# Performance work log

Measured on AMD Instinct MI355X. Metric: run time of the kernel, lower is better.

Reference implementation:

```python
import jax, jax.numpy as jnp
import numpy as np

N, CIN, H, W_ = 16, 64, 56, 56
COUT, K, STRIDE, PAD = 64, 3, 1, 1


def setup_inputs() -> dict:
    key = jax.random.key(0)
    k1, k2 = jax.random.split(key)
    x = jax.random.normal(k1, (N, CIN, H, W_), dtype=jnp.float32)
    adder = jax.random.normal(k2, (COUT, CIN, K, K), dtype=jnp.float32)
    return {"x": x, "adder": adder}


def reference(x, adder):
    # AdderNet 2d: out[n,co,h,w] = -sum_{ci,kh,kw} |patch(n,:,h,w) - adder[co]|
    n, c, h, w = x.shape
    co = adder.shape[0]
    # im2col: [N, C*K*K, Ho, Wo]; feature dim ordered (c, kh, kw), matching
    # torch.nn.functional.unfold and adder.reshape(Co, C*K*K).
    patches = jax.lax.conv_general_dilated_patches(
        x, filter_shape=(K, K), window_strides=(STRIDE, STRIDE),
        padding=((PAD, PAD), (PAD, PAD)))
    n_, ckk, ho, wo = patches.shape
    p = patches.reshape(n_, ckk, ho * wo)          # [N, CKK, L]
    w_col = adder.reshape(co, ckk)                 # [Co, CKK]

    def per_filter(wf):
        # wf: [CKK]; negative L1 distance of this filter to every patch
        return -jnp.sum(jnp.abs(p - wf[None, :, None]), axis=1)  # [N, L]

    # Sequential map over output channels avoids materializing the full
    # [Co, N, CKK, L] broadcast tensor (~7 GB); peak extra memory is one
    # [N, CKK, L] diff buffer per step.
    out = jax.lax.map(per_filter, w_col)           # [Co, N, L]
    out = out.transpose(1, 0, 2).reshape(n_, co, ho, wo)
    return out
```

## Files before the change

### kernel.cpp

```cpp
#include <hip/hip_runtime.h>

#define N_    16
#define CIN_  64
#define HW_   56
#define COUT_ 64
#define HP    58
#define HPSQ  (HP * HP)

typedef float f4u __attribute__((ext_vector_type(4), aligned(4)));

__global__ void pad_x_kernel(const float* __restrict__ x, float* __restrict__ xp) {
    int idx = blockIdx.x * 256 + threadIdx.x;
    const int total = N_ * CIN_ * HPSQ;
    if (idx >= total) return;
    int w  = idx % HP;
    int t  = idx / HP;
    int h  = t % HP;
    int nc = t / HP;
    float v = 0.f;
    if (h >= 1 && h <= HW_ && w >= 1 && w <= HW_)
        v = x[((size_t)nc * HW_ + (h - 1)) * HW_ + (w - 1)];
    xp[idx] = v;
}

__device__ __forceinline__ void load_tile(const float* __restrict__ xc,
                                          float (&buf)[9][9]) {
    #pragma unroll
    for (int r = 0; r < 9; ++r) {
        f4u a = *(const f4u*)(xc + r * HP);
        f4u b = *(const f4u*)(xc + r * HP + 4);
        float c = xc[r * HP + 8];
        buf[r][0] = a.x; buf[r][1] = a.y; buf[r][2] = a.z; buf[r][3] = a.w;
        buf[r][4] = b.x; buf[r][5] = b.y; buf[r][6] = b.z; buf[r][7] = b.w;
        buf[r][8] = c;
    }
}

__device__ __forceinline__ void compute_tile(const float* __restrict__ wci,
                                             const float (&buf)[9][9],
                                             float (&acc)[7][7]) {
    #pragma unroll
    for (int kh = 0; kh < 3; ++kh) {
        #pragma unroll
        for (int kw = 0; kw < 3; ++kw) {
            float wv = wci[kh * 3 + kw];
            #pragma unroll
            for (int oh = 0; oh < 7; ++oh)
                #pragma unroll
                for (int j = 0; j < 7; ++j)
                    acc[oh][j] += fabsf(buf[oh + kh][j + kw] - wv);
        }
    }
}

__global__ __launch_bounds__(128, 2) void adder_main_kernel(
    const float* __restrict__ xp, const float* __restrict__ wt,
    float* __restrict__ out) {
    __shared__ float red[64][49];

    int bid  = blockIdx.x;
    int n    = bid >> 6;
    int co   = bid & 63;
    int tid  = threadIdx.x;
    int wid  = tid >> 6;
    int lane = tid & 63;
    int tx   = lane & 7;
    int ty   = lane >> 3;
    int h0   = ty * 7;
    int w0   = tx * 7;

    const float* xbase = xp + (size_t)n * CIN_ * HPSQ + h0 * HP + w0;
    const float* wbase = wt + co * 576;

    float acc[7][7];
    #pragma unroll
    for (int oh = 0; oh < 7; ++oh)
        #pragma unroll
        for (int j = 0; j < 7; ++j) acc[oh][j] = 0.f;

    const int ci0 = wid * 32;
    for (int ci = ci0; ci < ci0 + 32; ++ci) {
        float buf[9][9];
        load_tile(xbase + (size_t)ci * HPSQ, buf);
        compute_tile(wbase + ci * 9, buf, acc);
    }

    if (wid == 1) {
        #pragma unroll
        for (int oh = 0; oh < 7; ++oh)
            #pragma unroll
            for (int j = 0; j < 7; ++j) red[lane][oh * 7 + j] = acc[oh][j];
    }
    __syncthreads();
    if (wid == 0) {
        float* ob = out + ((size_t)(n * COUT_ + co) * HW_ + h0) * HW_ + w0;
        #pragma unroll
        for (int oh = 0; oh < 7; ++oh)
            #pragma unroll
            for (int j = 0; j < 7; ++j)
                ob[oh * HW_ + j] = -(acc[oh][j] + red[lane][oh * 7 + j]);
    }
}

extern "C" void kernel_launch(void* const* d_in, const int* in_sizes, int n_in,
                              void* d_out, int out_size, void* d_ws, size_t ws_size,
                              hipStream_t stream) {
    const float* x     = (const float*)d_in[0];
    const float* adder = (const float*)d_in[1];
    float* out = (float*)d_out;

    float* xp = (float*)d_ws;

    const int padTotal = N_ * CIN_ * HPSQ;
    pad_x_kernel<<<(padTotal + 255) / 256, 256, 0, stream>>>(x, xp);
    adder_main_kernel<<<N_ * COUT_, 128, 0, stream>>>(xp, adder, out);
}
```

Baseline: 211.5 us.

## Split input channels across four wavefronts and interleave row loads with compute

New measurement: 187.8 us. 1.13x faster.

```diff
diff --git a/kernel.cpp b/kernel.cpp
--- a/kernel.cpp
+++ b/kernel.cpp
@@ -23,40 +23,10 @@
     xp[idx] = v;
 }
 
-__device__ __forceinline__ void load_tile(const float* __restrict__ xc,
-                                          float (&buf)[9][9]) {
-    #pragma unroll
-    for (int r = 0; r < 9; ++r) {
-        f4u a = *(const f4u*)(xc + r * HP);
-        f4u b = *(const f4u*)(xc + r * HP + 4);
-        float c = xc[r * HP + 8];
-        buf[r][0] = a.x; buf[r][1] = a.y; buf[r][2] = a.z; buf[r][3] = a.w;
-        buf[r][4] = b.x; buf[r][5] = b.y; buf[r][6] = b.z; buf[r][7] = b.w;
-        buf[r][8] = c;
-    }
-}
-
-__device__ __forceinline__ void compute_tile(const float* __restrict__ wci,
-                                             const float (&buf)[9][9],
-                                             float (&acc)[7][7]) {
-    #pragma unroll
-    for (int kh = 0; kh < 3; ++kh) {
-        #pragma unroll
-        for (int kw = 0; kw < 3; ++kw) {
-            float wv = wci[kh * 3 + kw];
-            #pragma unroll
-            for (int oh = 0; oh < 7; ++oh)
-                #pragma unroll
-                for (int j = 0; j < 7; ++j)
-                    acc[oh][j] += fabsf(buf[oh + kh][j + kw] - wv);
-        }
-    }
-}
-
-__global__ __launch_bounds__(128, 2) void adder_main_kernel(
+__global__ __launch_bounds__(256, 4) void adder_main_kernel(
     const float* __restrict__ xp, const float* __restrict__ wt,
     float* __restrict__ out) {
-    __shared__ float red[64][49];
+    __shared__ float red[3][64][49];
 
     int bid  = blockIdx.x;
     int n    = bid >> 6;
@@ -70,35 +40,68 @@
     int w0   = tx * 7;
 
     const float* xbase = xp + (size_t)n * CIN_ * HPSQ + h0 * HP + w0;
-    const float* wbase = wt + co * 576;
+    const float* wbase = wt + (size_t)co * 576;
 
-    float acc[7][7];
-    #pragma unroll
-    for (int oh = 0; oh < 7; ++oh)
+    float acc[7][7] = {};
+
+    const int ci0 = wid * 16;
+    for (int ci = ci0; ci < ci0 + 16; ++ci) {
+        const float* xc  = xbase + (size_t)ci * HPSQ;
+        const float* wci = wbase + ci * 9;
+        float w[9];
         #pragma unroll
-        for (int j = 0; j < 7; ++j) acc[oh][j] = 0.f;
+        for (int k = 0; k < 9; ++k) w[k] = wci[k];
 
-    const int ci0 = wid * 32;
-    for (int ci = ci0; ci < ci0 + 32; ++ci) {
         float buf[9][9];
-        load_tile(xbase + (size_t)ci * HPSQ, buf);
-        compute_tile(wbase + ci * 9, buf, acc);
+        #define LOADROW(r) { \
+            f4u a_ = *(const f4u*)(xc + (r) * HP);      \
+            f4u b_ = *(const f4u*)(xc + (r) * HP + 4);  \
+            buf[r][0] = a_.x; buf[r][1] = a_.y; buf[r][2] = a_.z; buf[r][3] = a_.w; \
+            buf[r][4] = b_.x; buf[r][5] = b_.y; buf[r][6] = b_.z; buf[r][7] = b_.w; \
+            buf[r][8] = xc[(r) * HP + 8]; }
+        #define COMP(oh) { \
+            _Pragma("unroll") \
+            for (int kh = 0; kh < 3; ++kh) { \
+                _Pragma("unroll") \
+                for (int kw = 0; kw < 3; ++kw) { \
+                    float wv = w[kh * 3 + kw]; \
+                    _Pragma("unroll") \
+                    for (int j = 0; j < 7; ++j) \
+                        acc[oh][j] += fabsf(buf[(oh) + kh][j + kw] - wv); \
+                } } }
+
+        LOADROW(0) LOADROW(1) LOADROW(2)
+        COMP(0)
+        LOADROW(3) COMP(1)
+        LOADROW(4) COMP(2)
+        LOADROW(5) COMP(3)
+        LOADROW(6) COMP(4)
+        LOADROW(7) COMP(5)
+        LOADROW(8) COMP(6)
+        #undef LOADROW
+        #undef COMP
     }
 
-    if (wid == 1) {
+    if (wid != 0) {
+        float* rp = &red[wid - 1][lane][0];
         #pragma unroll
         for (int oh = 0; oh < 7; ++oh)
             #pragma unroll
-            for (int j = 0; j < 7; ++j) red[lane][oh * 7 + j] = acc[oh][j];
+            for (int j = 0; j < 7; ++j) rp[oh * 7 + j] = acc[oh][j];
     }
     __syncthreads();
     if (wid == 0) {
-        float* ob = out + ((size_t)(n * COUT_ + co) * HW_ + h0) * HW_ + w0;
+        float* ob = out + (((size_t)(n * COUT_ + co)) * HW_ + h0) * HW_ + w0;
         #pragma unroll
         for (int oh = 0; oh < 7; ++oh)
             #pragma unroll
-            for (int j = 0; j < 7; ++j)
-                ob[oh * HW_ + j] = -(acc[oh][j] + red[lane][oh * 7 + j]);
+            for (int j = 0; j < 7; ++j) {
+                float s = acc[oh][j]
+                        + red[0][lane][oh * 7 + j]
+                        + red[1][lane][oh * 7 + j]
+                        + red[2][lane][oh * 7 + j];
+                ob[oh * HW_ + j] = -s;
+            }
     }
 }
 
@@ -113,5 +116,5 @@
 
     const int padTotal = N_ * CIN_ * HPSQ;
     pad_x_kernel<<<(padTotal + 255) / 256, 256, 0, stream>>>(x, xp);
-    adder_main_kernel<<<N_ * COUT_, 128, 0, stream>>>(xp, adder, out);
+    adder_main_kernel<<<N_ * COUT_, 256, 0, stream>>>(xp, adder, out);
 }
```
